# Kernel tuning notes

Measured on AMD Instinct MI355X. Metric: run time of the kernel, lower is better.

## Reference

```python
import jax, jax.numpy as jnp
import numpy as np

DIM = 1024
HEADS = 16
HEAD_DIM = DIM // HEADS
DFF = 4 * DIM
EPS = 1e-6


def _layernorm(x, scale, bias):
    mu = jnp.mean(x, axis=-1, keepdims=True)
    var = jnp.mean(jnp.square(x - mu), axis=-1, keepdims=True)
    return (x - mu) * jax.lax.rsqrt(var + EPS) * scale + bias


def setup_inputs() -> dict:
    key = jax.random.key(0)
    ks = jax.random.split(key, 8)
    d = {}
    d["x"] = jax.random.normal(ks[0], (4, 2048, DIM), dtype=jnp.float32)
    # LayerNorm params
    d["ln1_scale"] = jnp.ones((DIM,), jnp.float32)
    d["ln1_bias"] = jnp.zeros((DIM,), jnp.float32)
    d["ln2_scale"] = jnp.ones((DIM,), jnp.float32)
    d["ln2_bias"] = jnp.zeros((DIM,), jnp.float32)
    # Attention params
    d["qkv_w"] = jax.random.normal(ks[1], (DIM, 3 * DIM), jnp.float32) * (DIM ** -0.5)
    d["qkv_b"] = jnp.zeros((3 * DIM,), jnp.float32)
    d["proj_w"] = jax.random.normal(ks[2], (DIM, DIM), jnp.float32) * (DIM ** -0.5)
    d["proj_b"] = jnp.zeros((DIM,), jnp.float32)
    # MLP params
    d["fc1_w"] = jax.random.normal(ks[3], (DIM, DFF), jnp.float32) * (DIM ** -0.5)
    d["fc1_b"] = jnp.zeros((DFF,), jnp.float32)
    d["fc2_w"] = jax.random.normal(ks[4], (DFF, DIM), jnp.float32) * (DFF ** -0.5)
    d["fc2_b"] = jnp.zeros((DIM,), jnp.float32)
    return d


def reference(x, ln1_scale, ln1_bias, ln2_scale, ln2_bias,
              qkv_w, qkv_b, proj_w, proj_b,
              fc1_w, fc1_b, fc2_w, fc2_b):
    B, S, D = x.shape
    scale = HEAD_DIM ** -0.5

    # --- Attention sub-block (pre-LN) ---
    h = _layernorm(x, ln1_scale, ln1_bias)
    qkv = h @ qkv_w + qkv_b                                  # [B,S,3D]
    qkv = qkv.reshape(B, S, 3, HEADS, HEAD_DIM)
    qkv = qkv.transpose(2, 0, 3, 1, 4)                       # [3,B,H,S,hd]
    q, k, v = qkv[0], qkv[1], qkv[2]
    attn = jnp.einsum('bhqd,bhkd->bhqk', q, k) * scale       # [B,H,S,S]
    attn = jax.nn.softmax(attn, axis=-1)
    out = jnp.einsum('bhqk,bhkd->bhqd', attn, v)             # [B,H,S,hd]
    out = out.transpose(0, 2, 1, 3).reshape(B, S, D)
    out = out @ proj_w + proj_b
    x = x + out

    # --- MLP sub-block (pre-LN) ---
    h = _layernorm(x, ln2_scale, ln2_bias)
    h = jax.nn.gelu(h @ fc1_w + fc1_b)
    h = h @ fc2_w + fc2_b
    return x + h
```

## Files before the change

kernel.cpp:

```cpp
#include <hip/hip_runtime.h>
#include <hip/hip_bf16.h>

typedef __attribute__((ext_vector_type(4))) float f32x4;
typedef __attribute__((ext_vector_type(16))) float f32x16;
typedef __attribute__((ext_vector_type(8))) short bf16x8;

__device__ __forceinline__ unsigned short f2bf(float f) {
    return __bfloat16_as_ushort(__float2bfloat16(f));
}

typedef __attribute__((address_space(1))) const unsigned char* gas_ptr;
typedef __attribute__((address_space(3))) unsigned char* las_ptr;
__device__ __forceinline__ void gload16(const void* g, void* l) {
    __builtin_amdgcn_global_load_lds((gas_ptr)g, (las_ptr)l, 16, 0, 0);
}

__device__ __forceinline__ unsigned cvt_pk_bf16(float lo, float hi) {
    unsigned r;
    asm("v_cvt_pk_bf16_f32 %0, %1, %2" : "=v"(r) : "v"(lo), "v"(hi));
    return r;
}

__global__ __launch_bounds__(256) void ln_kernel(
    const float* __restrict__ x, const float* __restrict__ scale,
    const float* __restrict__ bias, unsigned short* __restrict__ out)
{
    int row = blockIdx.x;
    const float* xr = x + (size_t)row * 1024;
    int t = threadIdx.x;
    float4 v = ((const float4*)xr)[t];
    float s  = v.x + v.y + v.z + v.w;
    float ss = v.x*v.x + v.y*v.y + v.z*v.z + v.w*v.w;
    #pragma unroll
    for (int m = 32; m; m >>= 1) { s += __shfl_down(s, m); ss += __shfl_down(ss, m); }
    __shared__ float red[8];
    int wid = t >> 6;
    if ((t & 63) == 0) { red[wid*2] = s; red[wid*2+1] = ss; }
    __syncthreads();
    s  = red[0] + red[2] + red[4] + red[6];
    ss = red[1] + red[3] + red[5] + red[7];
    float mu  = s * (1.0f/1024.0f);
    float var = ss * (1.0f/1024.0f) - mu*mu;
    float inv = rsqrtf(var + 1e-6f);
    float4 sc = ((const float4*)scale)[t];
    float4 bi = ((const float4*)bias)[t];
    ushort4 o;
    o.x = f2bf((v.x - mu)*inv*sc.x + bi.x);
    o.y = f2bf((v.y - mu)*inv*sc.y + bi.y);
    o.z = f2bf((v.z - mu)*inv*sc.z + bi.z);
    o.w = f2bf((v.w - mu)*inv*sc.w + bi.w);
    ((ushort4*)(out + (size_t)row * 1024))[t] = o;
}

__global__ __launch_bounds__(256) void transpose_kernel(
    const float* __restrict__ W, unsigned short* __restrict__ Wt, int K, int N)
{
    __shared__ float tile[32][33];
    int n0 = blockIdx.x * 32, k0 = blockIdx.y * 32;
    int tx = threadIdx.x, ty = threadIdx.y;
    #pragma unroll
    for (int j = 0; j < 32; j += 8)
        tile[ty + j][tx] = W[(size_t)(k0 + ty + j) * N + n0 + tx];
    __syncthreads();
    #pragma unroll
    for (int j = 0; j < 32; j += 8)
        Wt[(size_t)(n0 + ty + j) * K + k0 + tx] = f2bf(tile[tx][ty + j]);
}

template<int EPI, int BN>
__global__ __launch_bounds__(512, 2) void gemm256_kernel(
    const unsigned short* __restrict__ A,
    const unsigned short* __restrict__ Bt,
    const float* __restrict__ bias,
    const float* __restrict__ res,
    void* __restrict__ out,
    unsigned short* __restrict__ vtout,
    int M, int N, int K)
{
    constexpr int BM = 256;
    constexpr int WARPS_N = (BN == 256) ? 4 : 2;
    constexpr int WM = (BN == 256) ? 128 : 64;
    constexpr int WN = 64;
    constexpr int MQ = WM / 64;
    constexpr int NF = WN / 16;
    constexpr int NB = BN / 64;

    __shared__ __align__(16) unsigned short Al[2][BM * 64];
    __shared__ __align__(16) unsigned short Bl[2][BN * 64];

    int t = threadIdx.x;
    int wid = t >> 6, lane = t & 63;
    int wr = wid / WARPS_N, wc = wid % WARPS_N;
    int l15 = lane & 15, lg = lane >> 4;

    int gx = gridDim.x;
    int nwg = gx * gridDim.y;
    int orig = blockIdx.y * gx + blockIdx.x;
    int cpx = nwg >> 3;
    int wg = (orig & 7) * cpx + (orig >> 3);
    int bx = wg % gx, by = wg / gx;
    int brow = by * BM, bcol = bx * BN;

    f32x4 acc[MQ * 4][NF] = {};

    int sr  = t >> 3;
    int scb = (t & 7) * 16;
    int sce = (scb ^ ((sr & 7) << 4)) >> 1;
    const size_t aoff = (size_t)(brow + sr) * K + sce;
    const size_t boff = (size_t)(bcol + sr) * K + sce;

    auto stage = [&](int b, int kt2) {
        int k0 = kt2 << 6;
        char* la = (char*)Al[b] + (wid << 10);
        char* lb = (char*)Bl[b] + (wid << 10);
        #pragma unroll
        for (int i = 0; i < 4; i++)
            gload16(A + aoff + (size_t)(i * 64) * K + k0, la + i * 8192);
        #pragma unroll
        for (int j = 0; j < NB; j++)
            gload16(Bt + boff + (size_t)(j * 64) * K + k0, lb + j * 8192);
    };

    stage(0, 0);
    asm volatile("s_waitcnt vmcnt(0)" ::: "memory");
    __builtin_amdgcn_s_barrier();

    int nk = K >> 6;
    int rsw = (l15 & 7) << 4;
    for (int kt = 0; kt < nk; kt++) {
        int cur = kt & 1;
        if (kt + 1 < nk) stage(cur ^ 1, kt + 1);

        const char* Ab = (const char*)Al[cur];
        const char* Bb = (const char*)Bl[cur];

        bf16x8 bfr[NF][2];
        #pragma unroll
        for (int nf = 0; nf < NF; nf++) {
            int rb = wc * WN + nf * 16 + l15;
            #pragma unroll
            for (int kk = 0; kk < 2; kk++)
                bfr[nf][kk] = *(const bf16x8*)(Bb + rb * 128 + ((kk * 64 + lg * 16) ^ rsw));
        }
        #pragma unroll
        for (int mq = 0; mq < MQ; mq++) {
            bf16x8 af[4][2];
            #pragma unroll
            for (int mf = 0; mf < 4; mf++) {
                int ra = wr * WM + mq * 64 + mf * 16 + l15;
                #pragma unroll
                for (int kk = 0; kk < 2; kk++)
                    af[mf][kk] = *(const bf16x8*)(Ab + ra * 128 + ((kk * 64 + lg * 16) ^ rsw));
            }
            __builtin_amdgcn_s_setprio(1);
            #pragma unroll
            for (int mf = 0; mf < 4; mf++)
                #pragma unroll
                for (int nf = 0; nf < NF; nf++)
                    #pragma unroll
                    for (int kk = 0; kk < 2; kk++)
                        acc[mq*4+mf][nf] = __builtin_amdgcn_mfma_f32_16x16x32_bf16(
                            af[mf][kk], bfr[nf][kk], acc[mq*4+mf][nf], 0, 0, 0);
            __builtin_amdgcn_s_setprio(0);
        }

        asm volatile("s_waitcnt vmcnt(0)" ::: "memory");
        __builtin_amdgcn_s_barrier();
    }

    #pragma unroll
    for (int mi = 0; mi < MQ * 4; mi++) {
        #pragma unroll
        for (int nf = 0; nf < NF; nf++) {
            int col = bcol + wc * WN + nf * 16 + l15;
            float bs = bias[col];
            #pragma unroll
            for (int r = 0; r < 4; r++) {
                int row = brow + wr * WM + mi * 16 + lg * 4 + r;
                size_t idx = (size_t)row * N + col;
                float v = acc[mi][nf][r] + bs;
                if (EPI == 1) {
                    ((float*)out)[idx] = v + res[idx];
                } else if (EPI == 2) {
                    float u = v + 0.044715f * v * v * v;
                    float e = __builtin_amdgcn_exp2f(-2.3022077f * u);
                    float g = v * __builtin_amdgcn_rcpf(1.0f + e);
                    ((unsigned short*)out)[idx] = f2bf(g);
                } else {
                    unsigned short bv = f2bf(v);
                    ((unsigned short*)out)[idx] = bv;
                    if (col >= 2048) {
                        int hd = col - 2048;
                        int b = row >> 11, s = row & 2047;
                        vtout[((size_t)((b << 4) + (hd >> 6)) * 64 + (hd & 63)) * 2048 + s] = bv;
                    }
                }
            }
        }
    }
}

__global__ __launch_bounds__(512, 2) void attn_kernel(
    const unsigned short* __restrict__ qkv, const unsigned short* __restrict__ vt,
    unsigned short* __restrict__ ctx)
{
    __shared__ unsigned short Kl[2][4096];
    __shared__ unsigned short Vl[2][4096];

    int t = threadIdx.x;
    int wid = t >> 6, lane = t & 63;
    int l31 = lane & 31, half = lane >> 5;
    int bh = blockIdx.y;
    int b = bh >> 4, h = bh & 15;
    int qr0 = blockIdx.x * 256 + wid * 32;

    const size_t qbase = (size_t)b * 2048 * 3072 + (size_t)h * 64;
    const unsigned short* vbase = vt + (size_t)bh * 64 * 2048;

    bf16x8 qf[4];
    #pragma unroll
    for (int ds = 0; ds < 4; ds++)
        qf[ds] = *(const bf16x8*)(qkv + qbase + (size_t)(qr0 + l31) * 3072 + ds*16 + half*8);

    f32x16 ot0 = {}, ot1 = {};
    float mrun = -1e30f, lrun = 0.0f;
    const float C = 0.125f * 1.44269504f;

    int srow = t >> 3;
    int ssw = ((t & 7) * 16) ^ ((srow & 7) << 4);
    const unsigned short* kg = qkv + qbase + 1024 + (size_t)srow * 3072 + (ssw >> 1);
    const unsigned short* vg = vbase + (size_t)srow * 2048 + (ssw >> 1);

    gload16(kg, (char*)Kl[0] + t * 16);
    gload16(vg, (char*)Vl[0] + t * 16);
    __syncthreads();

    int cur = 0;
    for (int kt = 0; kt < 32; kt++) {
        if (kt < 31) {
            gload16(kg + (size_t)(kt + 1) * 64 * 3072, (char*)Kl[cur ^ 1] + t * 16);
            gload16(vg + (kt + 1) * 64,               (char*)Vl[cur ^ 1] + t * 16);
        }

        const char* Kb = (const char*)Kl[cur];
        const char* Vb = (const char*)Vl[cur];
        int sw = (l31 & 7) << 4;

        f32x16 st0 = {}, st1 = {};
        __builtin_amdgcn_s_setprio(1);
        #pragma unroll
        for (int ds = 0; ds < 4; ds++) {
            int colb = ds*32 + half*16;
            bf16x8 k0 = *(const bf16x8*)(Kb + l31*128 + (colb ^ sw));
            bf16x8 k1 = *(const bf16x8*)(Kb + (32 + l31)*128 + (colb ^ sw));
            st0 = __builtin_amdgcn_mfma_f32_32x32x16_bf16(k0, qf[ds], st0, 0, 0, 0);
            st1 = __builtin_amdgcn_mfma_f32_32x32x16_bf16(k1, qf[ds], st1, 0, 0, 0);
        }
        __builtin_amdgcn_s_setprio(0);

        float mx = fmaxf(st0[0], st0[1]);
        #pragma unroll
        for (int r = 2; r < 16; r++) mx = fmaxf(mx, st0[r]);
        #pragma unroll
        for (int r = 0; r < 16; r++) mx = fmaxf(mx, st1[r]);
        mx = fmaxf(mx, __shfl_xor(mx, 32));
        float pm = mx * C;

        bool grow = pm > mrun + 11.5416f;
        if (__any(grow)) {
            float mn = fmaxf(mrun, pm);
            float corr = __builtin_amdgcn_exp2f(mrun - mn);
            mrun = mn;
            lrun *= corr;
            ot0 *= corr;
            ot1 *= corr;
        }

        unsigned w0[8], w1[8];
        float sum = 0.0f;
        {
            float e[16];
            #pragma unroll
            for (int r = 0; r < 16; r++) { e[r] = __builtin_amdgcn_exp2f(fmaf(st0[r], C, -mrun)); sum += e[r]; }
            #pragma unroll
            for (int p = 0; p < 8; p++) w0[p] = cvt_pk_bf16(e[2*p], e[2*p+1]);
            #pragma unroll
            for (int r = 0; r < 16; r++) { e[r] = __builtin_amdgcn_exp2f(fmaf(st1[r], C, -mrun)); sum += e[r]; }
            #pragma unroll
            for (int p = 0; p < 8; p++) w1[p] = cvt_pk_bf16(e[2*p], e[2*p+1]);
        }
        lrun += sum;

        __builtin_amdgcn_s_setprio(1);
        #pragma unroll
        for (int ks = 0; ks < 4; ks++) {
            union { unsigned u[4]; bf16x8 v; } pf;
            unsigned* w = (ks < 2) ? w0 : w1;
            int o4 = (ks & 1) * 4;
            pf.u[0] = w[o4 + 0]; pf.u[1] = w[o4 + 1]; pf.u[2] = w[o4 + 2]; pf.u[3] = w[o4 + 3];
            int lo = ks*32 + half*8;
            union { unsigned long long d[2]; bf16x8 v; } va, vb;
            va.d[0] = *(const unsigned long long*)(Vb + l31*128 + (lo ^ sw));
            va.d[1] = *(const unsigned long long*)(Vb + l31*128 + ((lo + 16) ^ sw));
            vb.d[0] = *(const unsigned long long*)(Vb + (32 + l31)*128 + (lo ^ sw));
            vb.d[1] = *(const unsigned long long*)(Vb + (32 + l31)*128 + ((lo + 16) ^ sw));
            ot0 = __builtin_amdgcn_mfma_f32_32x32x16_bf16(va.v, pf.v, ot0, 0, 0, 0);
            ot1 = __builtin_amdgcn_mfma_f32_32x32x16_bf16(vb.v, pf.v, ot1, 0, 0, 0);
        }
        __builtin_amdgcn_s_setprio(0);

        __syncthreads();
        cur ^= 1;
    }

    float ltot = lrun + __shfl_xor(lrun, 32);
    float rl = 1.0f / ltot;
    size_t cb = (size_t)b * 2048 * 1024 + (size_t)(qr0 + l31) * 1024 + (size_t)h * 64;
    #pragma unroll
    for (int r = 0; r < 16; r++) {
        int d = (r & 3) + 8 * (r >> 2) + 4 * half;
        ctx[cb + d]      = f2bf(ot0[r] * rl);
        ctx[cb + 32 + d] = f2bf(ot1[r] * rl);
    }
}

extern "C" void kernel_launch(void* const* d_in, const int* in_sizes, int n_in,
                              void* d_out, int out_size, void* d_ws, size_t ws_size,
                              hipStream_t stream) {
    const float* x      = (const float*)d_in[0];
    const float* ln1_s  = (const float*)d_in[1];
    const float* ln1_b  = (const float*)d_in[2];
    const float* ln2_s  = (const float*)d_in[3];
    const float* ln2_b  = (const float*)d_in[4];
    const float* qkv_w  = (const float*)d_in[5];
    const float* qkv_b  = (const float*)d_in[6];
    const float* proj_w = (const float*)d_in[7];
    const float* proj_b = (const float*)d_in[8];
    const float* fc1_w  = (const float*)d_in[9];
    const float* fc1_b  = (const float*)d_in[10];
    const float* fc2_w  = (const float*)d_in[11];
    const float* fc2_b  = (const float*)d_in[12];
    float* out = (float*)d_out;

    char* ws = (char*)d_ws;
    unsigned short* vtb  = (unsigned short*)(ws + 0);
    float*          x1   = (float*)(ws + 0);
    unsigned short* h    = (unsigned short*)(ws + (size_t)32 * 1024 * 1024);
    unsigned short* qkvb = (unsigned short*)(ws + (size_t)48 * 1024 * 1024);
    unsigned short* gbuf = (unsigned short*)(ws + (size_t)48 * 1024 * 1024);
    unsigned short* ctxb = (unsigned short*)(ws + (size_t)96 * 1024 * 1024);
    unsigned short* wT   = (unsigned short*)(ws + (size_t)112 * 1024 * 1024);

    dim3 tb(32, 8);

    transpose_kernel<<<dim3(96, 32), tb, 0, stream>>>(qkv_w, wT, 1024, 3072);
    ln_kernel<<<8192, 256, 0, stream>>>(x, ln1_s, ln1_b, h);
    gemm256_kernel<3,128><<<dim3(24, 32), 512, 0, stream>>>(h, wT, qkv_b, nullptr, qkvb, vtb, 8192, 3072, 1024);
    attn_kernel<<<dim3(8, 64), 512, 0, stream>>>(qkvb, vtb, ctxb);
    transpose_kernel<<<dim3(32, 32), tb, 0, stream>>>(proj_w, wT, 1024, 1024);
    gemm256_kernel<1,128><<<dim3(8, 32), 512, 0, stream>>>(ctxb, wT, proj_b, x, x1, nullptr, 8192, 1024, 1024);
    ln_kernel<<<8192, 256, 0, stream>>>(x1, ln2_s, ln2_b, h);
    transpose_kernel<<<dim3(128, 32), tb, 0, stream>>>(fc1_w, wT, 1024, 4096);
    gemm256_kernel<2,256><<<dim3(16, 32), 512, 0, stream>>>(h, wT, fc1_b, nullptr, gbuf, nullptr, 8192, 4096, 1024);
    transpose_kernel<<<dim3(32, 128), tb, 0, stream>>>(fc2_w, wT, 4096, 1024);
    gemm256_kernel<1,128><<<dim3(8, 32), 512, 0, stream>>>(gbuf, wT, fc2_b, x1, out, nullptr, 8192, 1024, 4096);
}
```

Before: 422.7 us.

## Triple-buffer GEMM shared-memory stages and unify on a 256x128 tile

After: 446.6 us. 1.06x slower.

```diff
diff --git a/kernel.cpp b/kernel.cpp
--- a/kernel.cpp
+++ b/kernel.cpp
@@ -67,7 +67,7 @@
         Wt[(size_t)(n0 + ty + j) * K + k0 + tx] = f2bf(tile[tx][ty + j]);
 }
 
-template<int EPI, int BN>
+template<int EPI>
 __global__ __launch_bounds__(512, 2) void gemm256_kernel(
     const unsigned short* __restrict__ A,
     const unsigned short* __restrict__ Bt,
@@ -78,19 +78,14 @@
     int M, int N, int K)
 {
     constexpr int BM = 256;
-    constexpr int WARPS_N = (BN == 256) ? 4 : 2;
-    constexpr int WM = (BN == 256) ? 128 : 64;
-    constexpr int WN = 64;
-    constexpr int MQ = WM / 64;
-    constexpr int NF = WN / 16;
-    constexpr int NB = BN / 64;
-
-    __shared__ __align__(16) unsigned short Al[2][BM * 64];
-    __shared__ __align__(16) unsigned short Bl[2][BN * 64];
+    constexpr int BN = 128;
+
+    __shared__ __align__(16) unsigned short Al[3][BM * 64];
+    __shared__ __align__(16) unsigned short Bl[3][BN * 64];
 
     int t = threadIdx.x;
     int wid = t >> 6, lane = t & 63;
-    int wr = wid / WARPS_N, wc = wid % WARPS_N;
+    int wr = wid >> 1, wc = wid & 1;
     int l15 = lane & 15, lg = lane >> 4;
 
     int gx = gridDim.x;
@@ -101,7 +96,7 @@
     int bx = wg % gx, by = wg / gx;
     int brow = by * BM, bcol = bx * BN;
 
-    f32x4 acc[MQ * 4][NF] = {};
+    f32x4 acc[4][4] = {};
 
     int sr  = t >> 3;
     int scb = (t & 7) * 16;
@@ -117,66 +112,69 @@
         for (int i = 0; i < 4; i++)
             gload16(A + aoff + (size_t)(i * 64) * K + k0, la + i * 8192);
         #pragma unroll
-        for (int j = 0; j < NB; j++)
+        for (int j = 0; j < 2; j++)
             gload16(Bt + boff + (size_t)(j * 64) * K + k0, lb + j * 8192);
     };
 
+    int nk = K >> 6;
     stage(0, 0);
-    asm volatile("s_waitcnt vmcnt(0)" ::: "memory");
+    __builtin_amdgcn_sched_barrier(0);
+    stage(1, 1);
+    asm volatile("s_waitcnt vmcnt(6)" ::: "memory");
     __builtin_amdgcn_s_barrier();
 
-    int nk = K >> 6;
     int rsw = (l15 & 7) << 4;
+    int cur = 0, nxt2 = 2;
     for (int kt = 0; kt < nk; kt++) {
-        int cur = kt & 1;
-        if (kt + 1 < nk) stage(cur ^ 1, kt + 1);
+        if (kt + 2 < nk) stage(nxt2, kt + 2);
 
         const char* Ab = (const char*)Al[cur];
         const char* Bb = (const char*)Bl[cur];
 
-        bf16x8 bfr[NF][2];
-        #pragma unroll
-        for (int nf = 0; nf < NF; nf++) {
-            int rb = wc * WN + nf * 16 + l15;
+        bf16x8 bfr[4][2];
+        #pragma unroll
+        for (int nf = 0; nf < 4; nf++) {
+            int rb = wc * 64 + nf * 16 + l15;
             #pragma unroll
             for (int kk = 0; kk < 2; kk++)
                 bfr[nf][kk] = *(const bf16x8*)(Bb + rb * 128 + ((kk * 64 + lg * 16) ^ rsw));
         }
-        #pragma unroll
-        for (int mq = 0; mq < MQ; mq++) {
-            bf16x8 af[4][2];
-            #pragma unroll
-            for (int mf = 0; mf < 4; mf++) {
-                int ra = wr * WM + mq * 64 + mf * 16 + l15;
+        bf16x8 af[4][2];
+        #pragma unroll
+        for (int mf = 0; mf < 4; mf++) {
+            int ra = wr * 64 + mf * 16 + l15;
+            #pragma unroll
+            for (int kk = 0; kk < 2; kk++)
+                af[mf][kk] = *(const bf16x8*)(Ab + ra * 128 + ((kk * 64 + lg * 16) ^ rsw));
+        }
+        __builtin_amdgcn_s_setprio(1);
+        #pragma unroll
+        for (int mf = 0; mf < 4; mf++)
+            #pragma unroll
+            for (int nf = 0; nf < 4; nf++)
                 #pragma unroll
                 for (int kk = 0; kk < 2; kk++)
-                    af[mf][kk] = *(const bf16x8*)(Ab + ra * 128 + ((kk * 64 + lg * 16) ^ rsw));
-            }
-            __builtin_amdgcn_s_setprio(1);
-            #pragma unroll
-            for (int mf = 0; mf < 4; mf++)
-                #pragma unroll
-                for (int nf = 0; nf < NF; nf++)
-                    #pragma unroll
-                    for (int kk = 0; kk < 2; kk++)
-                        acc[mq*4+mf][nf] = __builtin_amdgcn_mfma_f32_16x16x32_bf16(
-                            af[mf][kk], bfr[nf][kk], acc[mq*4+mf][nf], 0, 0, 0);
-            __builtin_amdgcn_s_setprio(0);
-        }
-
-        asm volatile("s_waitcnt vmcnt(0)" ::: "memory");
+                    acc[mf][nf] = __builtin_amdgcn_mfma_f32_16x16x32_bf16(
+                        af[mf][kk], bfr[nf][kk], acc[mf][nf], 0, 0, 0);
+        __builtin_amdgcn_s_setprio(0);
+
+        if (kt + 2 < nk)      asm volatile("s_waitcnt vmcnt(6)" ::: "memory");
+        else if (kt + 1 < nk) asm volatile("s_waitcnt vmcnt(0)" ::: "memory");
         __builtin_amdgcn_s_barrier();
+
+        cur  = (cur  == 2) ? 0 : cur  + 1;
+        nxt2 = (nxt2 == 2) ? 0 : nxt2 + 1;
     }
 
     #pragma unroll
-    for (int mi = 0; mi < MQ * 4; mi++) {
-        #pragma unroll
-        for (int nf = 0; nf < NF; nf++) {
-            int col = bcol + wc * WN + nf * 16 + l15;
+    for (int mi = 0; mi < 4; mi++) {
+        #pragma unroll
+        for (int nf = 0; nf < 4; nf++) {
+            int col = bcol + wc * 64 + nf * 16 + l15;
             float bs = bias[col];
             #pragma unroll
             for (int r = 0; r < 4; r++) {
-                int row = brow + wr * WM + mi * 16 + lg * 4 + r;
+                int row = brow + wr * 64 + mi * 16 + lg * 4 + r;
                 size_t idx = (size_t)row * N + col;
                 float v = acc[mi][nf][r] + bs;
                 if (EPI == 1) {
@@ -355,13 +353,13 @@
 
     transpose_kernel<<<dim3(96, 32), tb, 0, stream>>>(qkv_w, wT, 1024, 3072);
     ln_kernel<<<8192, 256, 0, stream>>>(x, ln1_s, ln1_b, h);
-    gemm256_kernel<3,128><<<dim3(24, 32), 512, 0, stream>>>(h, wT, qkv_b, nullptr, qkvb, vtb, 8192, 3072, 1024);
+    gemm256_kernel<3><<<dim3(24, 32), 512, 0, stream>>>(h, wT, qkv_b, nullptr, qkvb, vtb, 8192, 3072, 1024);
     attn_kernel<<<dim3(8, 64), 512, 0, stream>>>(qkvb, vtb, ctxb);
     transpose_kernel<<<dim3(32, 32), tb, 0, stream>>>(proj_w, wT, 1024, 1024);
-    gemm256_kernel<1,128><<<dim3(8, 32), 512, 0, stream>>>(ctxb, wT, proj_b, x, x1, nullptr, 8192, 1024, 1024);
+    gemm256_kernel<1><<<dim3(8, 32), 512, 0, stream>>>(ctxb, wT, proj_b, x, x1, nullptr, 8192, 1024, 1024);
     ln_kernel<<<8192, 256, 0, stream>>>(x1, ln2_s, ln2_b, h);
     transpose_kernel<<<dim3(128, 32), tb, 0, stream>>>(fc1_w, wT, 1024, 4096);
-    gemm256_kernel<2,256><<<dim3(16, 32), 512, 0, stream>>>(h, wT, fc1_b, nullptr, gbuf, nullptr, 8192, 4096, 1024);
+    gemm256_kernel<2><<<dim3(32, 32), 512, 0, stream>>>(h, wT, fc1_b, nullptr, gbuf, nullptr, 8192, 4096, 1024);
     transpose_kernel<<<dim3(32, 128), tb, 0, stream>>>(fc2_w, wT, 4096, 1024);
-    gemm256_kernel<1,128><<<dim3(8, 32), 512, 0, stream>>>(gbuf, wT, fc2_b, x1, out, nullptr, 8192, 1024, 4096);
-}
+    gemm256_kernel<1><<<dim3(8, 32), 512, 0, stream>>>(gbuf, wT, fc2_b, x1, out, nullptr, 8192, 1024, 4096);
+}
```
